# Kernel optimization log

Hardware: AMD Instinct MI355X
Metric: run time of the kernel (lower is better)

Reference implementation:

```python
import jax, jax.numpy as jnp
import numpy as np

HIDDEN = 768
INNER = 512
EPS = 1e-5


def setup_inputs() -> dict:
    key = jax.random.key(0)
    ks = jax.random.split(key, 6)
    B, S = 8, 4096
    x = jax.random.normal(ks[0], (B, S, HIDDEN), dtype=jnp.float32)
    W1 = jax.random.normal(ks[1], (INNER, HIDDEN), dtype=jnp.float32) * 0.02
    b1 = jnp.zeros((INNER,), dtype=jnp.float32)
    W2 = jax.random.normal(ks[2], (HIDDEN, INNER), dtype=jnp.float32) * 0.02
    b2 = jnp.zeros((HIDDEN,), dtype=jnp.float32)
    # output_proj: nn.Linear(hidden, hidden)
    bound = 1.0 / np.sqrt(HIDDEN)
    Wo = jax.random.uniform(ks[3], (HIDDEN, HIDDEN), minval=-bound, maxval=bound, dtype=jnp.float32)
    bo = jax.random.uniform(ks[4], (HIDDEN,), minval=-bound, maxval=bound, dtype=jnp.float32)
    # LayerNorm affine params
    gamma = jnp.ones((HIDDEN,), dtype=jnp.float32)
    beta = jnp.zeros((HIDDEN,), dtype=jnp.float32)
    return {"x": x, "W1": W1, "b1": b1, "W2": W2, "b2": b2,
            "Wo": Wo, "bo": bo, "gamma": gamma, "beta": beta}


def reference(x, W1, b1, W2, b2, Wo, bo, gamma, beta):
    # NOTE: the torch module's inner 'TTT update' loop never actually modifies
    # W1/b1/W2/b2 (loss computed, no step applied), so the math per token is
    # independent and fully vectorizable across (batch, seq).
    h = jax.nn.relu(jnp.einsum('bsd,id->bsi', x, W1) + b1)       # [B,S,INNER]
    pred = jnp.einsum('bsi,di->bsd', h, W2) + b2                 # [B,S,HIDDEN]
    out = jnp.einsum('bsd,ed->bse', pred, Wo) + bo               # output_proj
    # LayerNorm over last dim
    mu = jnp.mean(out, axis=-1, keepdims=True)
    var = jnp.mean(jnp.square(out - mu), axis=-1, keepdims=True)
    out = (out - mu) * jax.lax.rsqrt(var + EPS) * gamma + beta
    return out
```

## Files before the change

### kernel.cpp

```cpp
#include <hip/hip_runtime.h>
#include <hip/hip_bf16.h>


#define HIDDEN 768
#define INNER  512

typedef __bf16 bf16_t;
typedef bf16_t bf16x8 __attribute__((ext_vector_type(8)));
typedef bf16_t bf16x4 __attribute__((ext_vector_type(4)));
typedef float  f32x4  __attribute__((ext_vector_type(4)));

__device__ __forceinline__ void async16(const void* g, void* lds) {
  __builtin_amdgcn_global_load_lds(
      (const __attribute__((address_space(1))) unsigned int*)g,
      (__attribute__((address_space(3))) unsigned int*)lds, 16, 0, 0);
}

__global__ __launch_bounds__(256)
void prep(const float* __restrict__ x, const float* __restrict__ W1,
          const float* __restrict__ W2, const float* __restrict__ Wo,
          bf16_t* __restrict__ xb, bf16_t* __restrict__ W1b,
          bf16_t* __restrict__ W2t, bf16_t* __restrict__ Wob, int xb_blocks) {
  __shared__ float T[64][65];
  const int b = blockIdx.x, t = threadIdx.x;

  const float4* src; bf16x4* dst; int base;
  if (b < xb_blocks)            { src = (const float4*)x;  dst = (bf16x4*)xb;  base = b * 4096; }
  else if (b < xb_blocks + 24)  { src = (const float4*)W1; dst = (bf16x4*)W1b; base = (b - xb_blocks) * 4096; }
  else if (b < xb_blocks + 60)  { src = (const float4*)Wo; dst = (bf16x4*)Wob; base = (b - xb_blocks - 24) * 4096; }
  else {
    const int tile = b - xb_blocks - 60;
    const int d0 = (tile >> 3) << 6;
    const int i0 = (tile & 7) << 6;
#pragma unroll
    for (int j = 0; j < 4; ++j) {
      const int idx = j * 256 + t;
      const int r = idx >> 4, c4 = idx & 15;
      float4 v = *(const float4*)(W2 + (size_t)(d0 + r) * INNER + i0 + c4 * 4);
      T[r][c4 * 4 + 0] = v.x; T[r][c4 * 4 + 1] = v.y;
      T[r][c4 * 4 + 2] = v.z; T[r][c4 * 4 + 3] = v.w;
    }
    __syncthreads();
    const int i = t & 63, h4 = t >> 6;
    bf16x8 o0, o1;
#pragma unroll
    for (int c = 0; c < 8; ++c) { o0[c] = (bf16_t)T[h4 * 16 + c][i]; o1[c] = (bf16_t)T[h4 * 16 + 8 + c][i]; }
    bf16_t* orow = W2t + (size_t)(i0 + i) * HIDDEN + d0 + h4 * 16;
    *(bf16x8*)orow = o0;
    *(bf16x8*)(orow + 8) = o1;
    return;
  }
#pragma unroll
  for (int i = 0; i < 16; ++i) {
    float4 v = src[base + i * 256 + t];
    bf16x4 o;
    o[0] = (bf16_t)v.x; o[1] = (bf16_t)v.y; o[2] = (bf16_t)v.z; o[3] = (bf16_t)v.w;
    dst[base + i * 256 + t] = o;
  }
}

__global__ __launch_bounds__(256)
void beq_k(const float* __restrict__ Wo, const float* __restrict__ b2,
           const float* __restrict__ bo, float* __restrict__ beq) {
  const int e = blockIdx.x * 4 + (threadIdx.x >> 6);
  const int l = threadIdx.x & 63;
  float s = 0.f;
#pragma unroll
  for (int j = 0; j < 12; ++j) s += Wo[(size_t)e * HIDDEN + j * 64 + l] * b2[j * 64 + l];
#pragma unroll
  for (int off = 1; off < 64; off <<= 1) s += __shfl_xor(s, off, 64);
  if (l == 0) beq[e] = s + bo[e];
}

__global__ __launch_bounds__(256, 2)
void gemm_small(const bf16_t* __restrict__ A, const bf16_t* __restrict__ Bt,
                bf16_t* __restrict__ Cout) {
  constexpr int N_ = INNER, K_ = HIDDEN, NT = N_ / 128, T = K_ / 64;
  __shared__ __align__(16) bf16_t As[2][128 * 64];
  __shared__ __align__(16) bf16_t Bs[2][128 * 64];

  const int per = gridDim.x >> 3;
  const int nb  = (blockIdx.x & 7) * per + (blockIdx.x >> 3);
  const int m0 = (nb / NT) * 128;
  const int n0 = (nb % NT) * 128;

  const int tid = threadIdx.x;
  const int w = tid >> 6, l = tid & 63;
  const int wr = w >> 1, wc = w & 1;
  const int fr = l & 15, fq = l >> 4;

#define STAGE2(dst, src, r0, k0)                                              \
  _Pragma("unroll") for (int i = 0; i < 4; ++i) {                             \
    const int G = i * 256 + tid, row = G >> 3, g = G & 7;                     \
    async16((src) + (size_t)((r0) + row) * K_ + (k0) + ((g ^ (row & 7)) << 3),\
            (char*)(dst) + (size_t)(i * 256 + w * 64) * 16);                  \
  }

  STAGE2(As[0], A, m0, 0); STAGE2(Bs[0], Bt, n0, 0);
  __syncthreads();

  f32x4 acc[4][4] = {};
#pragma unroll
  for (int t = 0; t < T; ++t) {
    const int cur = t & 1;
    if (t < T - 1) {
      STAGE2(As[cur ^ 1], A, m0, (t + 1) * 64);
      STAGE2(Bs[cur ^ 1], Bt, n0, (t + 1) * 64);
    }
#pragma unroll
    for (int kk = 0; kk < 2; ++kk) {
      bf16x8 ax[4], bx[4];
#pragma unroll
      for (int m = 0; m < 4; ++m) {
        const int row = wr * 64 + m * 16 + fr;
        const int slot = (kk * 4 + fq) ^ (row & 7);
        ax[m] = *(const bf16x8*)((const char*)As[cur] + row * 128 + slot * 16);
      }
#pragma unroll
      for (int n = 0; n < 4; ++n) {
        const int row = wc * 64 + n * 16 + fr;
        const int slot = (kk * 4 + fq) ^ (row & 7);
        bx[n] = *(const bf16x8*)((const char*)Bs[cur] + row * 128 + slot * 16);
      }
#pragma unroll
      for (int m = 0; m < 4; ++m)
#pragma unroll
        for (int n = 0; n < 4; ++n)
          acc[m][n] = __builtin_amdgcn_mfma_f32_16x16x32_bf16(ax[m], bx[n], acc[m][n], 0, 0, 0);
    }
    __syncthreads();
  }
#undef STAGE2

  const int orow0 = m0 + wr * 64 + fq * 4;
  const int ocol0 = n0 + wc * 64 + fr;
#pragma unroll
  for (int n = 0; n < 4; ++n)
#pragma unroll
    for (int m = 0; m < 4; ++m)
#pragma unroll
      for (int j = 0; j < 4; ++j)
        Cout[(size_t)(orow0 + m * 16 + j) * N_ + ocol0 + n * 16] = (bf16_t)acc[m][n][j];
}

template <int N_, int K_, int MODE>
__global__ __launch_bounds__(512, 1)
void gemm_p3(const bf16_t* __restrict__ A, const bf16_t* __restrict__ Bt,
             const float* __restrict__ bias, bf16_t* __restrict__ Cout) {
  constexpr int NT = N_ / 256;
  constexpr int T  = K_ / 64;
  __shared__ __align__(16) bf16_t As[3][128 * 64];
  __shared__ __align__(16) bf16_t Bs[3][256 * 64];

  const int per = gridDim.x >> 3;
  const int nb  = (blockIdx.x & 7) * per + (blockIdx.x >> 3);
  const int m0 = (nb / NT) * 128;
  const int n0 = (nb % NT) * 256;

  const int tid = threadIdx.x;
  const int w = tid >> 6, l = tid & 63;
  const int wm = w >> 2, wn = w & 3;
  const int fr = l & 15, fq = l >> 4;

#define STAGE_A(buf, k0)                                                      \
  _Pragma("unroll") for (int i = 0; i < 2; ++i) {                             \
    const int G = i * 512 + tid, row = G >> 3, g = G & 7;                     \
    async16(A + (size_t)(m0 + row) * K_ + (k0) + ((g ^ (row & 7)) << 3),      \
            (char*)As[buf] + (size_t)(i * 512 + w * 64) * 16);                \
  }
#define STAGE_B(buf, k0)                                                      \
  _Pragma("unroll") for (int i = 0; i < 4; ++i) {                             \
    const int G = i * 512 + tid, row = G >> 3, g = G & 7;                     \
    async16(Bt + (size_t)(n0 + row) * K_ + (k0) + ((g ^ (row & 7)) << 3),     \
            (char*)Bs[buf] + (size_t)(i * 512 + w * 64) * 16);                \
  }

  STAGE_A(0, 0);  STAGE_B(0, 0);
  STAGE_A(1, 64); STAGE_B(1, 64);
  asm volatile("s_waitcnt vmcnt(6)" ::: "memory");
  __builtin_amdgcn_s_barrier();

  f32x4 acc[4][4] = {};
#pragma unroll
  for (int t = 0; t < T; ++t) {
    const int cur = t % 3;
    if (t + 2 < T) {
      const int nx = (t + 2) % 3;
      STAGE_A(nx, (t + 2) * 64);
      STAGE_B(nx, (t + 2) * 64);
    }
    __builtin_amdgcn_s_setprio(1);
#pragma unroll
    for (int kk = 0; kk < 2; ++kk) {
      bf16x8 ax[4], bx[4];
#pragma unroll
      for (int m = 0; m < 4; ++m) {
        const int row = wm * 64 + m * 16 + fr;
        const int slot = (kk * 4 + fq) ^ (row & 7);
        ax[m] = *(const bf16x8*)((const char*)As[cur] + row * 128 + slot * 16);
      }
#pragma unroll
      for (int n = 0; n < 4; ++n) {
        const int row = wn * 64 + n * 16 + fr;
        const int slot = (kk * 4 + fq) ^ (row & 7);
        bx[n] = *(const bf16x8*)((const char*)Bs[cur] + row * 128 + slot * 16);
      }
#pragma unroll
      for (int m = 0; m < 4; ++m)
#pragma unroll
        for (int n = 0; n < 4; ++n)
          acc[m][n] = __builtin_amdgcn_mfma_f32_16x16x32_bf16(ax[m], bx[n], acc[m][n], 0, 0, 0);
    }
    __builtin_amdgcn_s_setprio(0);
    if (t < T - 1) {
      if (t + 2 < T) asm volatile("s_waitcnt vmcnt(6)" ::: "memory");
      else           asm volatile("s_waitcnt vmcnt(0)" ::: "memory");
      __builtin_amdgcn_s_barrier();
    }
  }
#undef STAGE_A
#undef STAGE_B

  const int orow0 = m0 + wm * 64 + fq * 4;
  const int ocol0 = n0 + wn * 64 + fr;
#pragma unroll
  for (int n = 0; n < 4; ++n) {
    const int col = ocol0 + n * 16;
    const float bv = bias[col];
#pragma unroll
    for (int m = 0; m < 4; ++m)
#pragma unroll
      for (int j = 0; j < 4; ++j) {
        float v = acc[m][n][j] + bv;
        if (MODE == 0) v = fmaxf(v, 0.f);
        Cout[(size_t)(orow0 + m * 16 + j) * N_ + col] = (bf16_t)v;
      }
  }
}

__global__ __launch_bounds__(256)
void ln_bf16(const bf16_t* __restrict__ raw, const float* __restrict__ gamma,
             const float* __restrict__ beta, float* __restrict__ out) {
  const int r = blockIdx.x * 4 + (threadIdx.x >> 6);
  const int l = threadIdx.x & 63;
  const bf16_t* rp = raw + (size_t)r * HIDDEN;
  float v[12];
  float s = 0.f, q = 0.f;
#pragma unroll
  for (int c = 0; c < 3; ++c) {
    bf16x4 b4 = *(const bf16x4*)(rp + c * 256 + l * 4);
#pragma unroll
    for (int j = 0; j < 4; ++j) {
      const float f = (float)b4[j];
      v[c * 4 + j] = f; s += f; q += f * f;
    }
  }
#pragma unroll
  for (int off = 1; off < 64; off <<= 1) {
    s += __shfl_xor(s, off, 64);
    q += __shfl_xor(q, off, 64);
  }
  const float mu  = s * (1.0f / HIDDEN);
  const float var = fmaxf(q * (1.0f / HIDDEN) - mu * mu, 0.f);
  const float inv = rsqrtf(var + 1e-5f);
  float* op = out + (size_t)r * HIDDEN;
#pragma unroll
  for (int c = 0; c < 3; ++c) {
    float4 g = ((const float4*)gamma)[c * 64 + l];
    float4 b = ((const float4*)beta)[c * 64 + l];
    float4 o;
    o.x = (v[c * 4 + 0] - mu) * inv * g.x + b.x;
    o.y = (v[c * 4 + 1] - mu) * inv * g.y + b.y;
    o.z = (v[c * 4 + 2] - mu) * inv * g.z + b.z;
    o.w = (v[c * 4 + 3] - mu) * inv * g.w + b.w;
    ((float4*)op)[c * 64 + l] = o;
  }
}

extern "C" void kernel_launch(void* const* d_in, const int* in_sizes, int n_in,
                              void* d_out, int out_size, void* d_ws, size_t ws_size,
                              hipStream_t stream) {
  const float* x     = (const float*)d_in[0];
  const float* W1    = (const float*)d_in[1];
  const float* b1    = (const float*)d_in[2];
  const float* W2    = (const float*)d_in[3];
  const float* b2    = (const float*)d_in[4];
  const float* Wo    = (const float*)d_in[5];
  const float* bo    = (const float*)d_in[6];
  const float* gamma = (const float*)d_in[7];
  const float* beta  = (const float*)d_in[8];

  const int M = in_sizes[0] / HIDDEN;

  char* ws = (char*)d_ws;
  bf16_t* xb   = (bf16_t*)ws;
  bf16_t* raw  = xb;
  bf16_t* h    = (bf16_t*)(ws + (size_t)M * HIDDEN * 2);
  bf16_t* W1b  = (bf16_t*)(ws + (size_t)M * HIDDEN * 2 + (size_t)M * INNER * 2);
  bf16_t* W2t  = W1b + INNER * HIDDEN;
  bf16_t* Wob  = W2t + INNER * HIDDEN;
  bf16_t* Weq  = Wob + HIDDEN * HIDDEN;
  float*  beq  = (float*)(Weq + HIDDEN * INNER);

  const int xb_blocks = (M * HIDDEN / 4) / 4096;

  prep<<<xb_blocks + 60 + 96, 256, 0, stream>>>(x, W1, W2, Wo, xb, W1b, W2t, Wob, xb_blocks);
  beq_k<<<HIDDEN / 4, 256, 0, stream>>>(Wo, b2, bo, beq);

  gemm_small<<<(HIDDEN / 128) * (INNER / 128), 256, 0, stream>>>(Wob, W2t, Weq);
  gemm_p3<INNER, HIDDEN, 0><<<(M / 128) * (INNER / 256), 512, 0, stream>>>(xb, W1b, b1, h);
  gemm_p3<HIDDEN, INNER, 1><<<(M / 128) * (HIDDEN / 256), 512, 0, stream>>>(h, Weq, beq, raw);
  ln_bf16<<<M / 4, 256, 0, stream>>>(raw, gamma, beta, (float*)d_out);
}
```

Baseline: 144.7 us.

## Fuse fp32-to-bf16 conversion of x into first GEMM and retile GEMMs

Removes the separate pass converting x to bf16 by loading fp32 x tiles directly into LDS with an XOR swizzle and converting to bf16 when building MFMA fragments in the first GEMM. The first GEMM now uses 128x128 tiles with 256 threads and triple buffering, and the second GEMM switches to a double-buffered 128x128 256-thread kernel shared with the weight-fold GEMM. This cuts a full read and write of the bf16 copy of x, at the cost of doubled LDS traffic for the A operand, extra conversion instructions in the inner loop, and a smaller N tile that reloads A more often.

```diff
diff --git a/kernel.cpp b/kernel.cpp
--- a/kernel.cpp
+++ b/kernel.cpp
@@ -17,19 +17,17 @@
 }
 
 __global__ __launch_bounds__(256)
-void prep(const float* __restrict__ x, const float* __restrict__ W1,
-          const float* __restrict__ W2, const float* __restrict__ Wo,
-          bf16_t* __restrict__ xb, bf16_t* __restrict__ W1b,
-          bf16_t* __restrict__ W2t, bf16_t* __restrict__ Wob, int xb_blocks) {
+void prep(const float* __restrict__ W1, const float* __restrict__ W2,
+          const float* __restrict__ Wo, bf16_t* __restrict__ W1b,
+          bf16_t* __restrict__ W2t, bf16_t* __restrict__ Wob) {
   __shared__ float T[64][65];
   const int b = blockIdx.x, t = threadIdx.x;
 
   const float4* src; bf16x4* dst; int base;
-  if (b < xb_blocks)            { src = (const float4*)x;  dst = (bf16x4*)xb;  base = b * 4096; }
-  else if (b < xb_blocks + 24)  { src = (const float4*)W1; dst = (bf16x4*)W1b; base = (b - xb_blocks) * 4096; }
-  else if (b < xb_blocks + 60)  { src = (const float4*)Wo; dst = (bf16x4*)Wob; base = (b - xb_blocks - 24) * 4096; }
+  if (b < 24)       { src = (const float4*)W1; dst = (bf16x4*)W1b; base = b * 4096; }
+  else if (b < 60)  { src = (const float4*)Wo; dst = (bf16x4*)Wob; base = (b - 24) * 4096; }
   else {
-    const int tile = b - xb_blocks - 60;
+    const int tile = b - 60;
     const int d0 = (tile >> 3) << 6;
     const int i0 = (tile & 7) << 6;
 #pragma unroll
@@ -72,112 +70,39 @@
   if (l == 0) beq[e] = s + bo[e];
 }
 
-__global__ __launch_bounds__(256, 2)
-void gemm_small(const bf16_t* __restrict__ A, const bf16_t* __restrict__ Bt,
-                bf16_t* __restrict__ Cout) {
-  constexpr int N_ = INNER, K_ = HIDDEN, NT = N_ / 128, T = K_ / 64;
-  __shared__ __align__(16) bf16_t As[2][128 * 64];
-  __shared__ __align__(16) bf16_t Bs[2][128 * 64];
+__global__ __launch_bounds__(256, 1)
+void gemm1_fused(const float* __restrict__ x, const bf16_t* __restrict__ W1b,
+                 const float* __restrict__ b1, bf16_t* __restrict__ h) {
+  constexpr int T = HIDDEN / 64;
+  __shared__ __align__(16) float  Af[3][128 * 64];
+  __shared__ __align__(16) bf16_t Bs[3][128 * 64];
 
   const int per = gridDim.x >> 3;
   const int nb  = (blockIdx.x & 7) * per + (blockIdx.x >> 3);
-  const int m0 = (nb / NT) * 128;
-  const int n0 = (nb % NT) * 128;
+  const int m0  = (nb >> 2) * 128;
+  const int n0  = (nb & 3) * 128;
 
   const int tid = threadIdx.x;
   const int w = tid >> 6, l = tid & 63;
   const int wr = w >> 1, wc = w & 1;
   const int fr = l & 15, fq = l >> 4;
 
-#define STAGE2(dst, src, r0, k0)                                              \
+#define STAGE_A(buf, k0)                                                      \
+  _Pragma("unroll") for (int i = 0; i < 8; ++i) {                             \
+    const int G = i * 256 + tid, row = G >> 4, g = G & 15;                    \
+    async16(x + (size_t)(m0 + row) * HIDDEN + (k0) + ((g ^ (row & 15)) << 2), \
+            (char*)Af[buf] + (size_t)(i * 256 + w * 64) * 16);                \
+  }
+#define STAGE_B(buf, k0)                                                      \
   _Pragma("unroll") for (int i = 0; i < 4; ++i) {                             \
     const int G = i * 256 + tid, row = G >> 3, g = G & 7;                     \
-    async16((src) + (size_t)((r0) + row) * K_ + (k0) + ((g ^ (row & 7)) << 3),\
-            (char*)(dst) + (size_t)(i * 256 + w * 64) * 16);                  \
-  }
-
-  STAGE2(As[0], A, m0, 0); STAGE2(Bs[0], Bt, n0, 0);
-  __syncthreads();
-
-  f32x4 acc[4][4] = {};
-#pragma unroll
-  for (int t = 0; t < T; ++t) {
-    const int cur = t & 1;
-    if (t < T - 1) {
-      STAGE2(As[cur ^ 1], A, m0, (t + 1) * 64);
-      STAGE2(Bs[cur ^ 1], Bt, n0, (t + 1) * 64);
-    }
-#pragma unroll
-    for (int kk = 0; kk < 2; ++kk) {
-      bf16x8 ax[4], bx[4];
-#pragma unroll
-      for (int m = 0; m < 4; ++m) {
-        const int row = wr * 64 + m * 16 + fr;
-        const int slot = (kk * 4 + fq) ^ (row & 7);
-        ax[m] = *(const bf16x8*)((const char*)As[cur] + row * 128 + slot * 16);
-      }
-#pragma unroll
-      for (int n = 0; n < 4; ++n) {
-        const int row = wc * 64 + n * 16 + fr;
-        const int slot = (kk * 4 + fq) ^ (row & 7);
-        bx[n] = *(const bf16x8*)((const char*)Bs[cur] + row * 128 + slot * 16);
-      }
-#pragma unroll
-      for (int m = 0; m < 4; ++m)
-#pragma unroll
-        for (int n = 0; n < 4; ++n)
-          acc[m][n] = __builtin_amdgcn_mfma_f32_16x16x32_bf16(ax[m], bx[n], acc[m][n], 0, 0, 0);
-    }
-    __syncthreads();
-  }
-#undef STAGE2
-
-  const int orow0 = m0 + wr * 64 + fq * 4;
-  const int ocol0 = n0 + wc * 64 + fr;
-#pragma unroll
-  for (int n = 0; n < 4; ++n)
-#pragma unroll
-    for (int m = 0; m < 4; ++m)
-#pragma unroll
-      for (int j = 0; j < 4; ++j)
-        Cout[(size_t)(orow0 + m * 16 + j) * N_ + ocol0 + n * 16] = (bf16_t)acc[m][n][j];
-}
-
-template <int N_, int K_, int MODE>
-__global__ __launch_bounds__(512, 1)
-void gemm_p3(const bf16_t* __restrict__ A, const bf16_t* __restrict__ Bt,
-             const float* __restrict__ bias, bf16_t* __restrict__ Cout) {
-  constexpr int NT = N_ / 256;
-  constexpr int T  = K_ / 64;
-  __shared__ __align__(16) bf16_t As[3][128 * 64];
-  __shared__ __align__(16) bf16_t Bs[3][256 * 64];
-
-  const int per = gridDim.x >> 3;
-  const int nb  = (blockIdx.x & 7) * per + (blockIdx.x >> 3);
-  const int m0 = (nb / NT) * 128;
-  const int n0 = (nb % NT) * 256;
-
-  const int tid = threadIdx.x;
-  const int w = tid >> 6, l = tid & 63;
-  const int wm = w >> 2, wn = w & 3;
-  const int fr = l & 15, fq = l >> 4;
-
-#define STAGE_A(buf, k0)                                                      \
-  _Pragma("unroll") for (int i = 0; i < 2; ++i) {                             \
-    const int G = i * 512 + tid, row = G >> 3, g = G & 7;                     \
-    async16(A + (size_t)(m0 + row) * K_ + (k0) + ((g ^ (row & 7)) << 3),      \
-            (char*)As[buf] + (size_t)(i * 512 + w * 64) * 16);                \
-  }
-#define STAGE_B(buf, k0)                                                      \
-  _Pragma("unroll") for (int i = 0; i < 4; ++i) {                             \
-    const int G = i * 512 + tid, row = G >> 3, g = G & 7;                     \
-    async16(Bt + (size_t)(n0 + row) * K_ + (k0) + ((g ^ (row & 7)) << 3),     \
-            (char*)Bs[buf] + (size_t)(i * 512 + w * 64) * 16);                \
+    async16(W1b + (size_t)(n0 + row) * HIDDEN + (k0) + ((g ^ (row & 7)) << 3),\
+            (char*)Bs[buf] + (size_t)(i * 256 + w * 64) * 16);                \
   }
 
   STAGE_A(0, 0);  STAGE_B(0, 0);
   STAGE_A(1, 64); STAGE_B(1, 64);
-  asm volatile("s_waitcnt vmcnt(6)" ::: "memory");
+  asm volatile("s_waitcnt vmcnt(12)" ::: "memory");
   __builtin_amdgcn_s_barrier();
 
   f32x4 acc[4][4] = {};
@@ -195,13 +120,101 @@
       bf16x8 ax[4], bx[4];
 #pragma unroll
       for (int m = 0; m < 4; ++m) {
-        const int row = wm * 64 + m * 16 + fr;
+        const int row = wr * 64 + m * 16 + fr;
+        const int c0 = kk * 8 + fq * 2;
+        const int s0 = c0 ^ (row & 15), s1 = (c0 + 1) ^ (row & 15);
+        f32x4 p0 = *(const f32x4*)(Af[cur] + row * 64 + s0 * 4);
+        f32x4 p1 = *(const f32x4*)(Af[cur] + row * 64 + s1 * 4);
+        bf16x8 a;
+#pragma unroll
+        for (int c = 0; c < 4; ++c) { a[c] = (bf16_t)p0[c]; a[4 + c] = (bf16_t)p1[c]; }
+        ax[m] = a;
+      }
+#pragma unroll
+      for (int n = 0; n < 4; ++n) {
+        const int row = wc * 64 + n * 16 + fr;
+        const int slot = (kk * 4 + fq) ^ (row & 7);
+        bx[n] = *(const bf16x8*)((const char*)Bs[cur] + row * 128 + slot * 16);
+      }
+#pragma unroll
+      for (int m = 0; m < 4; ++m)
+#pragma unroll
+        for (int n = 0; n < 4; ++n)
+          acc[m][n] = __builtin_amdgcn_mfma_f32_16x16x32_bf16(ax[m], bx[n], acc[m][n], 0, 0, 0);
+    }
+    __builtin_amdgcn_s_setprio(0);
+    if (t < T - 1) {
+      if (t + 2 < T) asm volatile("s_waitcnt vmcnt(12)" ::: "memory");
+      else           asm volatile("s_waitcnt vmcnt(0)"  ::: "memory");
+      __builtin_amdgcn_s_barrier();
+    }
+  }
+#undef STAGE_A
+#undef STAGE_B
+
+  const int orow0 = m0 + wr * 64 + fq * 4;
+  const int ocol0 = n0 + wc * 64 + fr;
+#pragma unroll
+  for (int n = 0; n < 4; ++n) {
+    const int col = ocol0 + n * 16;
+    const float bv = b1[col];
+#pragma unroll
+    for (int m = 0; m < 4; ++m)
+#pragma unroll
+      for (int j = 0; j < 4; ++j)
+        h[(size_t)(orow0 + m * 16 + j) * INNER + col] = (bf16_t)fmaxf(acc[m][n][j] + bv, 0.f);
+  }
+}
+
+template <int N_, int K_, int MODE>
+__global__ __launch_bounds__(256, 2)
+void gemm_bt(const bf16_t* __restrict__ A, const bf16_t* __restrict__ Bt,
+             const float* __restrict__ bias, bf16_t* __restrict__ Cout) {
+  constexpr int NT = N_ / 128;
+  constexpr int T  = K_ / 64;
+  __shared__ __align__(16) bf16_t As[2][128 * 64];
+  __shared__ __align__(16) bf16_t Bs[2][128 * 64];
+
+  const int per = gridDim.x >> 3;
+  const int nb  = (blockIdx.x & 7) * per + (blockIdx.x >> 3);
+  const int m0 = (nb / NT) * 128;
+  const int n0 = (nb % NT) * 128;
+
+  const int tid = threadIdx.x;
+  const int w = tid >> 6, l = tid & 63;
+  const int wr = w >> 1, wc = w & 1;
+  const int fr = l & 15, fq = l >> 4;
+
+#define STAGE(dst, src, r0, k0)                                               \
+  _Pragma("unroll") for (int i = 0; i < 4; ++i) {                             \
+    const int G = i * 256 + tid, row = G >> 3, g = G & 7;                     \
+    async16((src) + (size_t)((r0) + row) * K_ + (k0) + ((g ^ (row & 7)) << 3),\
+            (char*)(dst) + (size_t)(i * 256 + w * 64) * 16);                  \
+  }
+
+  STAGE(As[0], A, m0, 0); STAGE(Bs[0], Bt, n0, 0);
+  __syncthreads();
+
+  f32x4 acc[4][4] = {};
+#pragma unroll
+  for (int t = 0; t < T; ++t) {
+    const int cur = t & 1;
+    if (t < T - 1) {
+      STAGE(As[cur ^ 1], A, m0, (t + 1) * 64);
+      STAGE(Bs[cur ^ 1], Bt, n0, (t + 1) * 64);
+    }
+#pragma unroll
+    for (int kk = 0; kk < 2; ++kk) {
+      bf16x8 ax[4], bx[4];
+#pragma unroll
+      for (int m = 0; m < 4; ++m) {
+        const int row = wr * 64 + m * 16 + fr;
         const int slot = (kk * 4 + fq) ^ (row & 7);
         ax[m] = *(const bf16x8*)((const char*)As[cur] + row * 128 + slot * 16);
       }
 #pragma unroll
       for (int n = 0; n < 4; ++n) {
-        const int row = wn * 64 + n * 16 + fr;
+        const int row = wc * 64 + n * 16 + fr;
         const int slot = (kk * 4 + fq) ^ (row & 7);
         bx[n] = *(const bf16x8*)((const char*)Bs[cur] + row * 128 + slot * 16);
       }
@@ -211,30 +224,21 @@
         for (int n = 0; n < 4; ++n)
           acc[m][n] = __builtin_amdgcn_mfma_f32_16x16x32_bf16(ax[m], bx[n], acc[m][n], 0, 0, 0);
     }
-    __builtin_amdgcn_s_setprio(0);
-    if (t < T - 1) {
-      if (t + 2 < T) asm volatile("s_waitcnt vmcnt(6)" ::: "memory");
-      else           asm volatile("s_waitcnt vmcnt(0)" ::: "memory");
-      __builtin_amdgcn_s_barrier();
-    }
-  }
-#undef STAGE_A
-#undef STAGE_B
-
-  const int orow0 = m0 + wm * 64 + fq * 4;
-  const int ocol0 = n0 + wn * 64 + fr;
+    __syncthreads();
+  }
+#undef STAGE
+
+  const int orow0 = m0 + wr * 64 + fq * 4;
+  const int ocol0 = n0 + wc * 64 + fr;
 #pragma unroll
   for (int n = 0; n < 4; ++n) {
     const int col = ocol0 + n * 16;
-    const float bv = bias[col];
+    const float bv = (MODE == 2) ? 0.f : bias[col];
 #pragma unroll
     for (int m = 0; m < 4; ++m)
 #pragma unroll
-      for (int j = 0; j < 4; ++j) {
-        float v = acc[m][n][j] + bv;
-        if (MODE == 0) v = fmaxf(v, 0.f);
-        Cout[(size_t)(orow0 + m * 16 + j) * N_ + col] = (bf16_t)v;
-      }
+      for (int j = 0; j < 4; ++j)
+        Cout[(size_t)(orow0 + m * 16 + j) * N_ + col] = (bf16_t)(acc[m][n][j] + bv);
   }
 }
 
@@ -293,8 +297,7 @@
   const int M = in_sizes[0] / HIDDEN;
 
   char* ws = (char*)d_ws;
-  bf16_t* xb   = (bf16_t*)ws;
-  bf16_t* raw  = xb;
+  bf16_t* raw  = (bf16_t*)ws;
   bf16_t* h    = (bf16_t*)(ws + (size_t)M * HIDDEN * 2);
   bf16_t* W1b  = (bf16_t*)(ws + (size_t)M * HIDDEN * 2 + (size_t)M * INNER * 2);
   bf16_t* W2t  = W1b + INNER * HIDDEN;
@@ -302,13 +305,11 @@
   bf16_t* Weq  = Wob + HIDDEN * HIDDEN;
   float*  beq  = (float*)(Weq + HIDDEN * INNER);
 
-  const int xb_blocks = (M * HIDDEN / 4) / 4096;
-
-  prep<<<xb_blocks + 60 + 96, 256, 0, stream>>>(x, W1, W2, Wo, xb, W1b, W2t, Wob, xb_blocks);
+  prep<<<156, 256, 0, stream>>>(W1, W2, Wo, W1b, W2t, Wob);
   beq_k<<<HIDDEN / 4, 256, 0, stream>>>(Wo, b2, bo, beq);
 
-  gemm_small<<<(HIDDEN / 128) * (INNER / 128), 256, 0, stream>>>(Wob, W2t, Weq);
-  gemm_p3<INNER, HIDDEN, 0><<<(M / 128) * (INNER / 256), 512, 0, stream>>>(xb, W1b, b1, h);
-  gemm_p3<HIDDEN, INNER, 1><<<(M / 128) * (HIDDEN / 256), 512, 0, stream>>>(h, Weq, beq, raw);
+  gemm_bt<INNER, HIDDEN, 2><<<(HIDDEN / 128) * (INNER / 128), 256, 0, stream>>>(Wob, W2t, nullptr, Weq);
+  gemm1_fused<<<(M / 128) * (INNER / 128), 256, 0, stream>>>(x, W1b, b1, h);
+  gemm_bt<HIDDEN, INNER, 1><<<(M / 128) * (HIDDEN / 128), 256, 0, stream>>>(h, Weq, beq, raw);
   ln_bf16<<<M / 4, 256, 0, stream>>>(raw, gamma, beta, (float*)d_out);
 }
```

Result: slower. 150.5 us (+4.0%).
